# Kernel tuning notes

Measured on AMD Instinct MI355X. Metric: run time of the kernel, lower is better.

## Reference

```python
import jax, jax.numpy as jnp
import numpy as np

N_NODES = 100000
N_EDGES = 3200000
F_IN = 256
N_CLASSES = 10


def setup_inputs() -> dict:
    key = jax.random.key(0)
    ks = jax.random.split(key, 10)
    x = jax.random.normal(ks[0], (N_NODES, F_IN), dtype=jnp.float32)
    edge_index = jax.random.randint(ks[1], (2, N_EDGES), 0, N_NODES, dtype=jnp.int64)
    def glorot(k, fan_in, fan_out):
        s = (6.0 / (fan_in + fan_out)) ** 0.5
        return jax.random.uniform(k, (fan_in, fan_out), jnp.float32, -s, s)
    return {
        "x": x,
        "edge_index": edge_index,
        "W_gcn": glorot(ks[2], F_IN, 64),
        "b_gcn": jnp.zeros((64,), jnp.float32),
        "W1": glorot(ks[3], 64, 32),
        "b1": jnp.zeros((32,), jnp.float32),
        "W2": glorot(ks[4], 32, 16),
        "b2": jnp.zeros((16,), jnp.float32),
        "W3": glorot(ks[5], 16, N_CLASSES),
        "b3": jnp.zeros((N_CLASSES,), jnp.float32),
    }


def gcn_conv(x, edge_index, W, b):
    # PyG GCNConv: x' = D^{-1/2} (A + I) D^{-1/2} (x W) + b, with self-loops.
    n = x.shape[0]
    loop = jnp.arange(n, dtype=edge_index.dtype)
    src = jnp.concatenate([edge_index[0], loop])  # [E+N]
    dst = jnp.concatenate([edge_index[1], loop])
    deg = jax.ops.segment_sum(jnp.ones(src.shape, jnp.float32), dst, num_segments=n)
    dinv = jnp.where(deg > 0, jax.lax.rsqrt(deg), 0.0)
    norm = dinv[src] * dinv[dst]  # [E+N]
    h = x @ W  # transform first (reduces message width to 64)
    msg = h[src] * norm[:, None]  # gather + scale
    out = jax.ops.segment_sum(msg, dst, num_segments=n)  # scatter-add
    return out + b


def reference(x, edge_index, W_gcn, b_gcn, W1, b1, W2, b2, W3, b3):
    # Dropout is a no-op in eval mode; reference uses deterministic eval math.
    h = jax.nn.relu(gcn_conv(x, edge_index, W_gcn, b_gcn))
    h = jax.nn.relu(h @ W1 + b1)
    h = jax.nn.relu(h @ W2 + b2)
    return h @ W3 + b3
```

## Files before the change

kernel.cpp:

```cpp
#include <hip/hip_runtime.h>

#define F_IN 256
#define CHUNK 8192

typedef short bf8_t __attribute__((ext_vector_type(8)));
typedef float f4_t  __attribute__((ext_vector_type(4)));

__device__ __forceinline__ unsigned short f2bf(float f) {
  unsigned u = __float_as_uint(f);
  unsigned r = (u + 0x7FFFu + ((u >> 16) & 1u)) >> 16;
  return (unsigned short)r;
}
#define BF_LO(d) __uint_as_float((d) << 16)
#define BF_HI(d) __uint_as_float((d) & 0xFFFF0000u)

__device__ __forceinline__ bf8_t pack8(float4 a, float4 b) {
  bf8_t r;
  r[0] = (short)f2bf(a.x); r[1] = (short)f2bf(a.y);
  r[2] = (short)f2bf(a.z); r[3] = (short)f2bf(a.w);
  r[4] = (short)f2bf(b.x); r[5] = (short)f2bf(b.y);
  r[6] = (short)f2bf(b.z); r[7] = (short)f2bf(b.w);
  return r;
}

__global__ __launch_bounds__(256) void wprep_kernel(
    const float* __restrict__ W, unsigned short* __restrict__ WbT) {
  const int i = blockIdx.x * 256 + threadIdx.x;
  const int k = i >> 6, n = i & 63;
  WbT[n * 256 + k] = f2bf(W[i]);
}

__global__ __launch_bounds__(256) void gemm_direct_kernel(
    const float* __restrict__ x, const unsigned short* __restrict__ WbT,
    const float* __restrict__ dinvp, unsigned short* __restrict__ hb, int M) {
  __shared__ short Bs[64][264];
  const int t = threadIdx.x;
  for (int i = t; i < 2048; i += 256) {
    const int n = i >> 5, kq = (i & 31) << 3;
    *(uint4*)&Bs[n][kq] = *(const uint4*)(WbT + n * 256 + kq);
  }
  __syncthreads();

  const int brow = blockIdx.x * 128;
  const int w = t >> 6;
  const int l = t & 63;
  const int ml = l & 15;
  const int quad = l >> 4;

  const int r0 = min(brow + w * 32 + ml, M - 1);
  const int r1 = min(brow + w * 32 + 16 + ml, M - 1);
  const float* xr0 = x + (size_t)r0 * F_IN + (quad << 3);
  const float* xr1 = x + (size_t)r1 * F_IN + (quad << 3);

  f4_t acc[2][4];
#pragma unroll
  for (int a = 0; a < 2; ++a)
#pragma unroll
    for (int b = 0; b < 4; ++b) acc[a][b] = (f4_t){0.f, 0.f, 0.f, 0.f};

#pragma unroll
  for (int k0 = 0; k0 < F_IN; k0 += 32) {
    bf8_t afr[2];
    {
      const float4 a0 = *(const float4*)(xr0 + k0);
      const float4 a1 = *(const float4*)(xr0 + k0 + 4);
      afr[0] = pack8(a0, a1);
      const float4 c0 = *(const float4*)(xr1 + k0);
      const float4 c1 = *(const float4*)(xr1 + k0 + 4);
      afr[1] = pack8(c0, c1);
    }
    bf8_t bfr[4];
#pragma unroll
    for (int nt = 0; nt < 4; ++nt)
      bfr[nt] = *(const bf8_t*)&Bs[nt * 16 + ml][k0 + (quad << 3)];
#pragma unroll
    for (int mt = 0; mt < 2; ++mt)
#pragma unroll
      for (int nt = 0; nt < 4; ++nt)
        acc[mt][nt] = __builtin_amdgcn_mfma_f32_16x16x32_bf16(
            afr[mt], bfr[nt], acc[mt][nt], 0, 0, 0);
  }

#pragma unroll
  for (int mt = 0; mt < 2; ++mt) {
#pragma unroll
    for (int reg = 0; reg < 4; ++reg) {
      const int row = brow + w * 32 + mt * 16 + (quad << 2) + reg;
      if (row < M) {
        const float di = dinvp[row];
#pragma unroll
        for (int nt = 0; nt < 4; ++nt)
          hb[(size_t)row * 64 + nt * 16 + ml] = f2bf(di * acc[mt][nt][reg]);
      }
    }
  }
}

__global__ __launch_bounds__(512) void sort_local_kernel(
    const int* __restrict__ src_arr, const int* __restrict__ dst_arr,
    int* __restrict__ espB, int* __restrict__ segStart, int* __restrict__ segCnt,
    int* __restrict__ bucketCount, int E, int NBK) {
  __shared__ int hist[512];
  __shared__ int s[512];
  __shared__ int cur[512];
  const int t = threadIdx.x;
  const int blk = blockIdx.x;
  const int base = blk * CHUNK;
  const int cnt = min(CHUNK, E - base);
  for (int i = t; i < NBK; i += 512) hist[i] = 0;
  __syncthreads();
  int pk[16], bk[16];
#pragma unroll
  for (int k = 0; k < 16; ++k) {
    const int i = t + k * 512;
    bk[k] = -1;
    if (i < cnt) {
      const int sv = src_arr[base + i];
      const int dv = dst_arr[base + i];
      pk[k] = sv | ((dv & 255) << 24);
      bk[k] = dv >> 8;
      atomicAdd(&hist[bk[k]], 1);
    }
  }
  __syncthreads();
  const int v = (t < NBK) ? hist[t] : 0;
  s[t] = v;
  __syncthreads();
#pragma unroll
  for (int off = 1; off < 512; off <<= 1) {
    int add = (t >= off) ? s[t - off] : 0;
    __syncthreads();
    s[t] += add;
    __syncthreads();
  }
  if (t < NBK) {
    const int excl = s[t] - v;
    cur[t] = excl;
    segStart[blk * NBK + t] = base + excl;
    segCnt[blk * NBK + t] = v;
    if (v) atomicAdd(&bucketCount[t], v);
  }
  __syncthreads();
#pragma unroll
  for (int k = 0; k < 16; ++k) {
    if (bk[k] >= 0) {
      const int pos = atomicAdd(&cur[bk[k]], 1);
      espB[base + pos] = pk[k];
    }
  }
}

__global__ __launch_bounds__(512) void scan_buckets_kernel(
    const int* __restrict__ bucketCount, int* __restrict__ bucketStart, int NBK) {
  __shared__ int s[512];
  const int t = threadIdx.x;
  const int v = (t < NBK) ? bucketCount[t] : 0;
  s[t] = v;
  __syncthreads();
#pragma unroll
  for (int off = 1; off < 512; off <<= 1) {
    int add = (t >= off) ? s[t - off] : 0;
    __syncthreads();
    s[t] += add;
    __syncthreads();
  }
  if (t < NBK) bucketStart[t] = s[t] - v;
  if (t == NBK - 1) bucketStart[NBK] = s[t];
}

__global__ __launch_bounds__(512) void fine_bin2_kernel(
    const int* __restrict__ espB, const int* __restrict__ segStart,
    const int* __restrict__ segCnt, const int* __restrict__ bucketStart,
    int* __restrict__ es, int* __restrict__ rowptr, float* __restrict__ dinvp,
    int N, int E, int NBK, int NCH) {
  __shared__ int segS[512];
  __shared__ int segC[512];
  __shared__ int sbuf[512];
  __shared__ int hist[256];
  __shared__ int cur[256];
  const int t = threadIdx.x;
  const int b = blockIdx.x;
  for (int i = t; i < 512; i += 512) { segS[i] = 0; segC[i] = 0; }
  if (t < 256) hist[t] = 0;
  __syncthreads();
  for (int i = t; i < NCH; i += 512) {
    segS[i] = segStart[i * NBK + b];
    segC[i] = segCnt[i * NBK + b];
  }
  __syncthreads();

  const int wid = t >> 6;
  const int lane = t & 63;

  for (int seg = wid; seg < NCH; seg += 8) {
    const int sS = segS[seg], c = segC[seg];
    for (int j = lane; j < c; j += 64)
      atomicAdd(&hist[((unsigned)espB[sS + j]) >> 24], 1);
  }
  __syncthreads();

  int v2 = 0;
  if (t < 256) { v2 = hist[t]; sbuf[t] = v2; }
  __syncthreads();
#pragma unroll
  for (int off = 1; off < 256; off <<= 1) {
    int add = 0;
    if (t < 256 && t >= off) add = sbuf[t - off];
    __syncthreads();
    if (t < 256) sbuf[t] += add;
    __syncthreads();
  }
  const int base = bucketStart[b];
  if (t < 256) {
    const int excl = sbuf[t] - v2;
    cur[t] = base + excl;
    const int node = b * 256 + t;
    if (node < N) {
      rowptr[node] = base + excl;
      dinvp[node] = rsqrtf((float)(v2 + 1));
    }
  }
  if (b == 0 && t == 0) rowptr[N] = E;
  __syncthreads();

  for (int seg = wid; seg < NCH; seg += 8) {
    const int sS = segS[seg], c = segC[seg];
    for (int j = lane; j < c; j += 64) {
      const int p = espB[sS + j];
      const int pos = atomicAdd(&cur[((unsigned)p) >> 24], 1);
      es[pos] = p & 0x00FFFFFF;
    }
  }
}

__global__ __launch_bounds__(256) void agg_csr_kernel(
    const unsigned short* __restrict__ hb, const int* __restrict__ es,
    const int* __restrict__ rowptr, const float* __restrict__ dinvp,
    float* __restrict__ agg, int N) {
  const int t = threadIdx.x;
  const int node = blockIdx.x * 4 + (t >> 6);
  if (node >= N) return;
  const int lane = t & 63;
  const int slot = lane >> 3;
  const int fq = (lane & 7) << 3;
  const int start = rowptr[node];
  const int end = rowptr[node + 1];

  float acc[8] = {0.f};
  int i = start + slot;
  for (; i + 8 < end; i += 16) {
    const int s0 = es[i];
    const int s1 = es[i + 8];
    const uint4 r0 = *(const uint4*)(hb + (size_t)s0 * 64 + fq);
    const uint4 r1 = *(const uint4*)(hb + (size_t)s1 * 64 + fq);
    acc[0] += BF_LO(r0.x) + BF_LO(r1.x);
    acc[1] += BF_HI(r0.x) + BF_HI(r1.x);
    acc[2] += BF_LO(r0.y) + BF_LO(r1.y);
    acc[3] += BF_HI(r0.y) + BF_HI(r1.y);
    acc[4] += BF_LO(r0.z) + BF_LO(r1.z);
    acc[5] += BF_HI(r0.z) + BF_HI(r1.z);
    acc[6] += BF_LO(r0.w) + BF_LO(r1.w);
    acc[7] += BF_HI(r0.w) + BF_HI(r1.w);
  }
  if (i < end) {
    const int s0 = es[i];
    const uint4 r0 = *(const uint4*)(hb + (size_t)s0 * 64 + fq);
    acc[0] += BF_LO(r0.x);
    acc[1] += BF_HI(r0.x);
    acc[2] += BF_LO(r0.y);
    acc[3] += BF_HI(r0.y);
    acc[4] += BF_LO(r0.z);
    acc[5] += BF_HI(r0.z);
    acc[6] += BF_LO(r0.w);
    acc[7] += BF_HI(r0.w);
  }
#pragma unroll
  for (int m = 8; m <= 32; m <<= 1)
#pragma unroll
    for (int j = 0; j < 8; ++j) acc[j] += __shfl_xor(acc[j], m, 64);

  if (slot == 0) {
    const float di = dinvp[node];
    float4 o0 = make_float4(acc[0] * di, acc[1] * di, acc[2] * di, acc[3] * di);
    float4 o1 = make_float4(acc[4] * di, acc[5] * di, acc[6] * di, acc[7] * di);
    float* ap = agg + (size_t)node * 64 + fq;
    *(float4*)(ap + 0) = o0;
    *(float4*)(ap + 4) = o1;
  }
}

__global__ __launch_bounds__(256) void mlp_mfma_kernel(
    const float* __restrict__ agg, const unsigned short* __restrict__ hb,
    const float* __restrict__ dinvp, const float* __restrict__ bg,
    const float* __restrict__ W1, const float* __restrict__ b1,
    const float* __restrict__ W2, const float* __restrict__ b2,
    const float* __restrict__ W3, const float* __restrict__ b3,
    float* __restrict__ out, int N) {
  __shared__ short g64[256 * 72];
  __shared__ short h2s[256 * 40];
  __shared__ short W1s[32 * 72];
  __shared__ short W2s[16 * 40];
  __shared__ short W3s[16 * 40];
  __shared__ float bgs[64], b1s[32], b2s[16], b3s[16];
  short* h1s = g64;

  const int t = threadIdx.x;
  const int node0 = blockIdx.x * 256;
  for (int i = t; i < 256 * 40; i += 256) h2s[i] = 0;
  for (int i = t; i < 16 * 40; i += 256) W3s[i] = 0;
  if (t < 64) bgs[t] = bg[t];
  if (t < 32) b1s[t] = b1[t];
  if (t < 16) { b2s[t] = b2[t]; b3s[t] = (t < 10) ? b3[t] : 0.f; }
  __syncthreads();
  for (int i = t; i < 2048; i += 256) { const int k = i >> 5, n = i & 31; W1s[n * 72 + k] = (short)f2bf(W1[i]); }
  for (int i = t; i < 512;  i += 256) { const int k = i >> 4, n = i & 15; W2s[n * 40 + k] = (short)f2bf(W2[i]); }
  if (t < 160) { const int k = t / 10, n = t % 10; W3s[n * 40 + k] = (short)f2bf(W3[t]); }
  {
    const int nd = min(node0 + t, N - 1);
    const float di = dinvp[nd];
    short* gr = &g64[t * 72];
    const float* ar = agg + (size_t)nd * 64;
    const unsigned short* hr = hb + (size_t)nd * 64;
#pragma unroll
    for (int k = 0; k < 64; k += 8) {
      const float4 a0 = *(const float4*)(ar + k);
      const float4 a1 = *(const float4*)(ar + k + 4);
      const uint4 r = *(const uint4*)(hr + k);
      gr[k + 0] = (short)f2bf(fmaxf(a0.x + di * BF_LO(r.x) + bgs[k + 0], 0.f));
      gr[k + 1] = (short)f2bf(fmaxf(a0.y + di * BF_HI(r.x) + bgs[k + 1], 0.f));
      gr[k + 2] = (short)f2bf(fmaxf(a0.z + di * BF_LO(r.y) + bgs[k + 2], 0.f));
      gr[k + 3] = (short)f2bf(fmaxf(a0.w + di * BF_HI(r.y) + bgs[k + 3], 0.f));
      gr[k + 4] = (short)f2bf(fmaxf(a1.x + di * BF_LO(r.z) + bgs[k + 4], 0.f));
      gr[k + 5] = (short)f2bf(fmaxf(a1.y + di * BF_HI(r.z) + bgs[k + 5], 0.f));
      gr[k + 6] = (short)f2bf(fmaxf(a1.z + di * BF_LO(r.w) + bgs[k + 6], 0.f));
      gr[k + 7] = (short)f2bf(fmaxf(a1.w + di * BF_HI(r.w) + bgs[k + 7], 0.f));
    }
  }
  __syncthreads();

  const int w = t >> 6;
  const int lane = t & 63;
  const int ml = lane & 15;
  const int quad = lane >> 4;

  bf8_t a1f[4][2], b1f[2][2];
#pragma unroll
  for (int mt = 0; mt < 4; ++mt)
#pragma unroll
    for (int ks = 0; ks < 2; ++ks)
      a1f[mt][ks] = *(const bf8_t*)&g64[(w * 64 + mt * 16 + ml) * 72 + ks * 32 + quad * 8];
#pragma unroll
  for (int nt = 0; nt < 2; ++nt)
#pragma unroll
    for (int ks = 0; ks < 2; ++ks)
      b1f[nt][ks] = *(const bf8_t*)&W1s[(nt * 16 + ml) * 72 + ks * 32 + quad * 8];
  f4_t acc1[4][2];
#pragma unroll
  for (int mt = 0; mt < 4; ++mt)
#pragma unroll
    for (int nt = 0; nt < 2; ++nt) acc1[mt][nt] = (f4_t){0.f, 0.f, 0.f, 0.f};
#pragma unroll
  for (int ks = 0; ks < 2; ++ks)
#pragma unroll
    for (int mt = 0; mt < 4; ++mt)
#pragma unroll
      for (int nt = 0; nt < 2; ++nt)
        acc1[mt][nt] = __builtin_amdgcn_mfma_f32_16x16x32_bf16(
            a1f[mt][ks], b1f[nt][ks], acc1[mt][nt], 0, 0, 0);
  __syncthreads();
#pragma unroll
  for (int mt = 0; mt < 4; ++mt)
#pragma unroll
    for (int nt = 0; nt < 2; ++nt)
#pragma unroll
      for (int reg = 0; reg < 4; ++reg) {
        const int row = w * 64 + mt * 16 + quad * 4 + reg;
        const int col = nt * 16 + ml;
        h1s[row * 40 + col] = (short)f2bf(fmaxf(acc1[mt][nt][reg] + b1s[col], 0.f));
      }
  __syncthreads();

  bf8_t a2f[4];
#pragma unroll
  for (int mt = 0; mt < 4; ++mt)
    a2f[mt] = *(const bf8_t*)&h1s[(w * 64 + mt * 16 + ml) * 40 + quad * 8];
  const bf8_t b2f = *(const bf8_t*)&W2s[ml * 40 + quad * 8];
  f4_t acc2[4];
#pragma unroll
  for (int mt = 0; mt < 4; ++mt) {
    acc2[mt] = (f4_t){0.f, 0.f, 0.f, 0.f};
    acc2[mt] = __builtin_amdgcn_mfma_f32_16x16x32_bf16(a2f[mt], b2f, acc2[mt], 0, 0, 0);
  }
  __syncthreads();
#pragma unroll
  for (int mt = 0; mt < 4; ++mt)
#pragma unroll
    for (int reg = 0; reg < 4; ++reg) {
      const int row = w * 64 + mt * 16 + quad * 4 + reg;
      h2s[row * 40 + ml] = (short)f2bf(fmaxf(acc2[mt][reg] + b2s[ml], 0.f));
    }
  __syncthreads();

  bf8_t a3f[4];
#pragma unroll
  for (int mt = 0; mt < 4; ++mt)
    a3f[mt] = *(const bf8_t*)&h2s[(w * 64 + mt * 16 + ml) * 40 + quad * 8];
  const bf8_t b3f = *(const bf8_t*)&W3s[ml * 40 + quad * 8];
#pragma unroll
  for (int mt = 0; mt < 4; ++mt) {
    f4_t acc3 = (f4_t){0.f, 0.f, 0.f, 0.f};
    acc3 = __builtin_amdgcn_mfma_f32_16x16x32_bf16(a3f[mt], b3f, acc3, 0, 0, 0);
#pragma unroll
    for (int reg = 0; reg < 4; ++reg) {
      const int node = node0 + w * 64 + mt * 16 + quad * 4 + reg;
      if (ml < 10 && node < N) out[(size_t)node * 10 + ml] = acc3[reg] + b3s[ml];
    }
  }
}

extern "C" void kernel_launch(void* const* d_in, const int* in_sizes, int n_in,
                              void* d_out, int out_size, void* d_ws, size_t ws_size,
                              hipStream_t stream) {
  const float* x     = (const float*)d_in[0];
  const int*   ei    = (const int*)d_in[1];
  const float* W_gcn = (const float*)d_in[2];
  const float* b_gcn = (const float*)d_in[3];
  const float* W1    = (const float*)d_in[4];
  const float* b1    = (const float*)d_in[5];
  const float* W2    = (const float*)d_in[6];
  const float* b2    = (const float*)d_in[7];
  const float* W3    = (const float*)d_in[8];
  const float* b3    = (const float*)d_in[9];
  float* out = (float*)d_out;

  const int N = in_sizes[0] / F_IN;
  const int E = in_sizes[1] / 2;
  const int* src = ei;
  const int* dst = ei + E;
  const int NBK = (N + 255) >> 8;
  const int NCH = (E + CHUNK - 1) / CHUNK;

  unsigned short* hb = (unsigned short*)d_ws;
  float* dinvp       = (float*)(hb + (size_t)N * 64);
  int*   es          = (int*)(dinvp + N);
  int*   rowptr      = es + E;
  int*   bucketCount = rowptr + N + 16;
  int*   bucketStart = bucketCount + 512;
  int*   espB        = bucketStart + 528;
  int*   segStart    = espB + E;
  int*   segCnt      = segStart + NCH * NBK;
  unsigned short* WbT= (unsigned short*)(segCnt + NCH * NBK);
  float* agg         = (float*)espB;

  hipMemsetAsync(bucketCount, 0, 512 * sizeof(int), stream);

  wprep_kernel<<<64, 256, 0, stream>>>(W_gcn, WbT);
  sort_local_kernel<<<NCH, 512, 0, stream>>>(
      src, dst, espB, segStart, segCnt, bucketCount, E, NBK);
  scan_buckets_kernel<<<1, 512, 0, stream>>>(bucketCount, bucketStart, NBK);
  fine_bin2_kernel<<<NBK, 512, 0, stream>>>(
      espB, segStart, segCnt, bucketStart, es, rowptr, dinvp, N, E, NBK, NCH);

  gemm_direct_kernel<<<(N + 127) / 128, 256, 0, stream>>>(x, WbT, dinvp, hb, N);

  agg_csr_kernel<<<(N + 3) / 4, 256, 0, stream>>>(hb, es, rowptr, dinvp, agg, N);

  mlp_mfma_kernel<<<(N + 255) / 256, 256, 0, stream>>>(
      agg, hb, dinvp, b_gcn, W1, b1, W2, b2, W3, b3, out, N);
}
```

Measured before the change: 344.0 us.

## Fuse GCN epilogue into aggregation and narrow fine-bin segment parallelism

Moves the self-loop, normalization, bias, ReLU and bf16 packing from the MLP kernel into the aggregation kernel. The intermediate is now written as bf16 (128 B/node) instead of fp32 agg (256 B/node), and the MLP no longer rereads hb and dinvp. The fine binning kernel also switches from 8 wavefronts over segments to 32 groups of 16 lanes, which gives more parallel segments in flight. Lanes per segment drop and the epilogue adds a few loads to the aggregation tail.

Measured after the change: 325.2 us. 5.5% less time.

```diff
diff --git a/kernel.cpp b/kernel.cpp
--- a/kernel.cpp
+++ b/kernel.cpp
@@ -180,7 +180,8 @@
   __shared__ int cur[256];
   const int t = threadIdx.x;
   const int b = blockIdx.x;
-  for (int i = t; i < 512; i += 512) { segS[i] = 0; segC[i] = 0; }
+  segS[t] = 0;
+  segC[t] = 0;
   if (t < 256) hist[t] = 0;
   __syncthreads();
   for (int i = t; i < NCH; i += 512) {
@@ -189,12 +190,12 @@
   }
   __syncthreads();
 
-  const int wid = t >> 6;
-  const int lane = t & 63;
-
-  for (int seg = wid; seg < NCH; seg += 8) {
+  const int sw = t >> 4;
+  const int sl = t & 15;
+
+  for (int seg = sw; seg < NCH; seg += 32) {
     const int sS = segS[seg], c = segC[seg];
-    for (int j = lane; j < c; j += 64)
+    for (int j = sl; j < c; j += 16)
       atomicAdd(&hist[((unsigned)espB[sS + j]) >> 24], 1);
   }
   __syncthreads();
@@ -223,9 +224,9 @@
   if (b == 0 && t == 0) rowptr[N] = E;
   __syncthreads();
 
-  for (int seg = wid; seg < NCH; seg += 8) {
+  for (int seg = sw; seg < NCH; seg += 32) {
     const int sS = segS[seg], c = segC[seg];
-    for (int j = lane; j < c; j += 64) {
+    for (int j = sl; j < c; j += 16) {
       const int p = espB[sS + j];
       const int pos = atomicAdd(&cur[((unsigned)p) >> 24], 1);
       es[pos] = p & 0x00FFFFFF;
@@ -233,10 +234,10 @@
   }
 }
 
-__global__ __launch_bounds__(256) void agg_csr_kernel(
+__global__ __launch_bounds__(256) void agg_fuse_kernel(
     const unsigned short* __restrict__ hb, const int* __restrict__ es,
     const int* __restrict__ rowptr, const float* __restrict__ dinvp,
-    float* __restrict__ agg, int N) {
+    const float* __restrict__ bg, unsigned short* __restrict__ g, int N) {
   const int t = threadIdx.x;
   const int node = blockIdx.x * 4 + (t >> 6);
   if (node >= N) return;
@@ -281,17 +282,25 @@
 
   if (slot == 0) {
     const float di = dinvp[node];
-    float4 o0 = make_float4(acc[0] * di, acc[1] * di, acc[2] * di, acc[3] * di);
-    float4 o1 = make_float4(acc[4] * di, acc[5] * di, acc[6] * di, acc[7] * di);
-    float* ap = agg + (size_t)node * 64 + fq;
-    *(float4*)(ap + 0) = o0;
-    *(float4*)(ap + 4) = o1;
+    const uint4 r = *(const uint4*)(hb + (size_t)node * 64 + fq);
+    const float4 bq0 = *(const float4*)(bg + fq);
+    const float4 bq1 = *(const float4*)(bg + fq + 4);
+    float4 v0 = make_float4(
+        fmaxf(di * (acc[0] + BF_LO(r.x)) + bq0.x, 0.f),
+        fmaxf(di * (acc[1] + BF_HI(r.x)) + bq0.y, 0.f),
+        fmaxf(di * (acc[2] + BF_LO(r.y)) + bq0.z, 0.f),
+        fmaxf(di * (acc[3] + BF_HI(r.y)) + bq0.w, 0.f));
+    float4 v1 = make_float4(
+        fmaxf(di * (acc[4] + BF_LO(r.z)) + bq1.x, 0.f),
+        fmaxf(di * (acc[5] + BF_HI(r.z)) + bq1.y, 0.f),
+        fmaxf(di * (acc[6] + BF_LO(r.w)) + bq1.z, 0.f),
+        fmaxf(di * (acc[7] + BF_HI(r.w)) + bq1.w, 0.f));
+    *(bf8_t*)(g + (size_t)node * 64 + fq) = pack8(v0, v1);
   }
 }
 
 __global__ __launch_bounds__(256) void mlp_mfma_kernel(
-    const float* __restrict__ agg, const unsigned short* __restrict__ hb,
-    const float* __restrict__ dinvp, const float* __restrict__ bg,
+    const unsigned short* __restrict__ g,
     const float* __restrict__ W1, const float* __restrict__ b1,
     const float* __restrict__ W2, const float* __restrict__ b2,
     const float* __restrict__ W3, const float* __restrict__ b3,
@@ -301,40 +310,23 @@
   __shared__ short W1s[32 * 72];
   __shared__ short W2s[16 * 40];
   __shared__ short W3s[16 * 40];
-  __shared__ float bgs[64], b1s[32], b2s[16], b3s[16];
+  __shared__ float b1s[32], b2s[16], b3s[16];
   short* h1s = g64;
 
   const int t = threadIdx.x;
   const int node0 = blockIdx.x * 256;
   for (int i = t; i < 256 * 40; i += 256) h2s[i] = 0;
   for (int i = t; i < 16 * 40; i += 256) W3s[i] = 0;
-  if (t < 64) bgs[t] = bg[t];
   if (t < 32) b1s[t] = b1[t];
   if (t < 16) { b2s[t] = b2[t]; b3s[t] = (t < 10) ? b3[t] : 0.f; }
   __syncthreads();
   for (int i = t; i < 2048; i += 256) { const int k = i >> 5, n = i & 31; W1s[n * 72 + k] = (short)f2bf(W1[i]); }
   for (int i = t; i < 512;  i += 256) { const int k = i >> 4, n = i & 15; W2s[n * 40 + k] = (short)f2bf(W2[i]); }
   if (t < 160) { const int k = t / 10, n = t % 10; W3s[n * 40 + k] = (short)f2bf(W3[t]); }
-  {
-    const int nd = min(node0 + t, N - 1);
-    const float di = dinvp[nd];
-    short* gr = &g64[t * 72];
-    const float* ar = agg + (size_t)nd * 64;
-    const unsigned short* hr = hb + (size_t)nd * 64;
-#pragma unroll
-    for (int k = 0; k < 64; k += 8) {
-      const float4 a0 = *(const float4*)(ar + k);
-      const float4 a1 = *(const float4*)(ar + k + 4);
-      const uint4 r = *(const uint4*)(hr + k);
-      gr[k + 0] = (short)f2bf(fmaxf(a0.x + di * BF_LO(r.x) + bgs[k + 0], 0.f));
-      gr[k + 1] = (short)f2bf(fmaxf(a0.y + di * BF_HI(r.x) + bgs[k + 1], 0.f));
-      gr[k + 2] = (short)f2bf(fmaxf(a0.z + di * BF_LO(r.y) + bgs[k + 2], 0.f));
-      gr[k + 3] = (short)f2bf(fmaxf(a0.w + di * BF_HI(r.y) + bgs[k + 3], 0.f));
-      gr[k + 4] = (short)f2bf(fmaxf(a1.x + di * BF_LO(r.z) + bgs[k + 4], 0.f));
-      gr[k + 5] = (short)f2bf(fmaxf(a1.y + di * BF_HI(r.z) + bgs[k + 5], 0.f));
-      gr[k + 6] = (short)f2bf(fmaxf(a1.z + di * BF_LO(r.w) + bgs[k + 6], 0.f));
-      gr[k + 7] = (short)f2bf(fmaxf(a1.w + di * BF_HI(r.w) + bgs[k + 7], 0.f));
-    }
+  for (int i = t; i < 2048; i += 256) {
+    const int row = i >> 3, q = (i & 7) << 3;
+    const int nd = min(node0 + row, N - 1);
+    *(uint4*)&g64[row * 72 + q] = *(const uint4*)(g + (size_t)nd * 64 + q);
   }
   __syncthreads();
 
@@ -450,7 +442,7 @@
   int*   segStart    = espB + E;
   int*   segCnt      = segStart + NCH * NBK;
   unsigned short* WbT= (unsigned short*)(segCnt + NCH * NBK);
-  float* agg         = (float*)espB;
+  unsigned short* g  = (unsigned short*)espB;
 
   hipMemsetAsync(bucketCount, 0, 512 * sizeof(int), stream);
 
@@ -463,8 +455,9 @@
 
   gemm_direct_kernel<<<(N + 127) / 128, 256, 0, stream>>>(x, WbT, dinvp, hb, N);
 
-  agg_csr_kernel<<<(N + 3) / 4, 256, 0, stream>>>(hb, es, rowptr, dinvp, agg, N);
+  agg_fuse_kernel<<<(N + 3) / 4, 256, 0, stream>>>(
+      hb, es, rowptr, dinvp, b_gcn, g, N);
 
   mlp_mfma_kernel<<<(N + 255) / 256, 256, 0, stream>>>(
-      agg, hb, dinvp, b_gcn, W1, b1, W2, b2, W3, b3, out, N);
-}
+      g, W1, b1, W2, b2, W3, b3, out, N);
+}
```
